# Optimization experiments

Hardware: AMD Instinct MI355X
Metric: run time of the kernel (lower is better)

The kernel has to match this reference:

```python
import jax, jax.numpy as jnp
import numpy as np
import math

H, C = 16, 4


def _clustering(x, alv, mu, log_var, log_prior, mi_estimation):
    # x: [B,h,L,D], alv: [B,h,L], mu/log_var: [h or 1, C, D], log_prior: [h or 1, C]
    B, Hh, L, D = x.shape
    z = x  # eval mode: no reparameterization noise
    zd = z[:, :, :, None, :]                       # [B,h,L,1,D]
    mu_b = mu[:, None, :, :]                       # [h,1,C,D]
    lv = log_var[:, None, :, :]
    var = jnp.exp(lv)
    lp = jax.nn.log_softmax(log_prior, axis=-1)    # [h,C]
    mse = (zd - mu_b) ** 2 / var                   # [B,h,L,C,D]
    log_pdf = -0.5 * mse.sum(-1) - 0.5 * lv.sum(-1) - D * math.pi  # [B,h,L,C]
    log_pdf = log_pdf + lp[:, None, :]
    shift = jax.lax.stop_gradient(log_pdf.max(axis=-1, keepdims=True))
    log_probs = jax.nn.log_softmax(log_pdf - shift + 5.0, axis=-1)
    cp = jnp.exp(log_probs)                        # cluster probs [B,h,L,C]
    lp_b = jnp.broadcast_to(lp[None, :, None, :], log_probs.shape)
    # F.kl_div(log_probs, prior) = prior * (log prior - log_probs)
    kl = (jnp.exp(lp_b) * (lp_b - log_probs)).sum(-1).mean(axis=(1, 2))
    alv5 = alv[:, :, :, None, None]
    avar = jnp.exp(alv5)
    kl = kl + 0.5 * (cp * (mse + avar / var + lv).sum(-1)).sum(-1).mean(axis=(1, 2))
    kl = kl - 0.5 * ((1.0 + alv5).sum(-1) * D).mean(axis=(1, 2, 3))
    eye = jnp.eye(L, dtype=x.dtype)
    div = jnp.einsum('bhqc,bhkc->bhqk', cp, cp)
    div = ((div - eye) ** 2) * (eye * 1.25 + (1.0 - eye) * 0.75)
    div_loss = div.mean(axis=(1, 2, 3))
    if mi_estimation:
        pdf = jnp.exp(log_pdf - jax.lax.stop_gradient(log_pdf.max())).sum(-1, keepdims=True)
        w = cp * pdf
        mi_probs = w / jnp.maximum(w.sum(axis=2, keepdims=True), 1e-6)  # L1 normalize over L
        mi_p = jnp.minimum(jnp.einsum('bilc,bjlc->blij', mi_probs, cp), 1.0)
        mask_h = 1.0 - jnp.eye(Hh, dtype=x.dtype)
        mi_loss = -(jnp.log(1.0 - mi_p + 1e-6) * mask_h).mean(axis=(1, 2, 3)) * 10.0
        aff = jnp.einsum('bhqc,bhkc->bhqk', cp, cp)
        diag = jnp.diagonal(jax.nn.log_softmax(aff, axis=-1), axis1=2, axis2=3)
        mi_loss = mi_loss - diag.mean(axis=(1, 2))
    else:
        mi_loss = jnp.zeros_like(kl)
    return z, cp, kl, div_loss, mi_loss


def _forward(query, key, value, Wq, bq, Wk, bk, Wv, bv, Wo, bo, Wsem, bsem,
             Whead, bhead, tok_mu, tok_log_var, tok_log_prior,
             head_mu, head_log_var, head_log_prior):
    B, L, D = query.shape
    Dk = D // H
    q = query @ Wq + bq
    k = key @ Wk + bk
    v = value @ Wv + bv
    alv = (q @ Wsem + bsem).transpose(0, 2, 1)                 # [B,H,L]
    qh = q.reshape(B, L, H, Dk).transpose(0, 2, 1, 3)          # [B,H,L,Dk]
    z, cp_q, kl_q, div_q, _ = _clustering(qh, alv, tok_mu, tok_log_var, tok_log_prior, False)
    kh = k.reshape(B, L, H, Dk).transpose(0, 2, 1, 3)
    vh = v.reshape(B, L, H, Dk).transpose(0, 2, 1, 3)
    cluster_mask = jnp.einsum('bhqc,bhkc->bhqk', cp_q, cp_q)   # token-cluster affinity mask
    scores = jnp.einsum('bhqd,bhkd->bhqk', z, kh) / math.sqrt(Dk)
    attn = jax.nn.softmax(scores, axis=-1) * cluster_mask
    attn = attn / (attn.sum(axis=-1, keepdims=True) + 1e-6)
    ctx = jnp.einsum('bhqk,bhkd->bhqd', attn, vh)              # [B,H,L,Dk]
    ctx_f = ctx.transpose(0, 2, 1, 3).reshape(B, L, D)
    alv_h = (ctx_f @ Whead + bhead).transpose(0, 2, 1)         # [B,H,L]
    _, cp_h, kl_h, div_h, mi = _clustering(ctx, alv_h, head_mu, head_log_var, head_log_prior, True)
    out = ctx_f @ Wo + bo
    return out, attn.mean(axis=1), kl_q + kl_h, div_q + div_h, mi


def setup_inputs() -> dict:
    key = jax.random.key(0)
    ks = jax.random.split(key, 12)
    B, L, D = 8, 512, 1024
    Dk = D // H
    s = 1.0 / math.sqrt(D)
    f32 = jnp.float32
    inp = {
        'query': jax.random.normal(ks[0], (B, L, D), f32),
        'key': jax.random.normal(ks[1], (B, L, D), f32),
        'value': jax.random.normal(ks[2], (B, L, D), f32),
        'Wq': jax.random.normal(ks[3], (D, D), f32) * s, 'bq': jnp.zeros((D,), f32),
        'Wk': jax.random.normal(ks[4], (D, D), f32) * s, 'bk': jnp.zeros((D,), f32),
        'Wv': jax.random.normal(ks[5], (D, D), f32) * s, 'bv': jnp.zeros((D,), f32),
        'Wo': jax.random.normal(ks[6], (D, D), f32) * s, 'bo': jnp.zeros((D,), f32),
        'Wsem': jax.random.normal(ks[7], (D, H), f32) * s, 'bsem': jnp.zeros((H,), f32),
        'Whead': jax.random.normal(ks[8], (D, H), f32) * s, 'bhead': jnp.zeros((H,), f32),
        'tok_mu': jax.random.normal(ks[9], (H, C, Dk), f32) * 0.1,
        'tok_log_var': jnp.zeros((H, C, Dk), f32),
        'tok_log_prior': jnp.full((H, C), math.log(1.0 / C), f32),
        'head_mu': jax.random.normal(ks[10], (1, C, Dk), f32) * 0.1,
        'head_log_var': jnp.zeros((1, C, Dk), f32),
        'head_log_prior': jnp.full((1, C), math.log(1.0 / C), f32),
    }
    return inp


def reference(query, key, value, Wq, bq, Wk, bk, Wv, bv, Wo, bo, Wsem, bsem,
              Whead, bhead, tok_mu, tok_log_var, tok_log_prior,
              head_mu, head_log_var, head_log_prior):
    return _forward(query, key, value, Wq, bq, Wk, bk, Wv, bv, Wo, bo, Wsem, bsem,
                    Whead, bhead, tok_mu, tok_log_var, tok_log_prior,
                    head_mu, head_log_var, head_log_prior)
```

## Files before the change

### kernel.cpp

```cpp
#include <hip/hip_runtime.h>
#include <math.h>

#define BB 8
#define LL 512
#define DD 1024
#define HH 16
#define CC 4
#define DK 64
#define NEG_DPI 201.06192982974676f

typedef __attribute__((ext_vector_type(8))) short short8;
typedef __attribute__((ext_vector_type(4))) float floatx4;
typedef __attribute__((ext_vector_type(8))) unsigned short u16x8;
typedef __attribute__((ext_vector_type(4))) unsigned short u16x4;

__device__ inline float block_sum256(float v, float* s_red) {
    int t = threadIdx.x;
    s_red[t] = v; __syncthreads();
    for (int off = 128; off > 0; off >>= 1) {
        if (t < off) s_red[t] += s_red[t + off];
        __syncthreads();
    }
    float r = s_red[0]; __syncthreads();
    return r;
}
__device__ inline float block_max256(float v, float* s_red) {
    int t = threadIdx.x;
    s_red[t] = v; __syncthreads();
    for (int off = 128; off > 0; off >>= 1) {
        if (t < off) s_red[t] = fmaxf(s_red[t], s_red[t + off]);
        __syncthreads();
    }
    float r = s_red[0]; __syncthreads();
    return r;
}
__device__ inline unsigned int fenc(float f) {
    unsigned int b = __float_as_uint(f);
    return (b & 0x80000000u) ? ~b : (b | 0x80000000u);
}
__device__ inline float fdec(unsigned int u) {
    return (u & 0x80000000u) ? __uint_as_float(u ^ 0x80000000u) : __uint_as_float(~u);
}
__device__ inline unsigned short f2bf(float x) {
    unsigned int u = __float_as_uint(x);
    return (unsigned short)((u + 0x7FFFu + ((u >> 16) & 1u)) >> 16);
}
__device__ inline unsigned short f2bf_cvt(float x) {
    __bf16 b = (__bf16)x;
    return __builtin_bit_cast(unsigned short, b);
}
__device__ inline float bf2f(unsigned short h) {
    return __uint_as_float((unsigned int)h << 16);
}
__device__ inline void split8(const float4 x, const float4 y, u16x8& h, u16x8& l) {
    float c[8] = {x.x, x.y, x.z, x.w, y.x, y.y, y.z, y.w};
    unsigned short hb[8];
#pragma unroll
    for (int j = 0; j < 8; j++) { hb[j] = f2bf_cvt(c[j]); h[j] = hb[j]; }
#pragma unroll
    for (int j = 0; j < 8; j++) c[j] = c[j] - bf2f(hb[j]);
#pragma unroll
    for (int j = 0; j < 8; j++) l[j] = f2bf_cvt(c[j]);
}

__global__ __launch_bounds__(256)
void wconv4(const float* __restrict__ W0, const float* __restrict__ W1,
            const float* __restrict__ W2, const float* __restrict__ W3,
            unsigned short* __restrict__ Tbase) {
    __shared__ float tile[64][65];
    int z = blockIdx.z;
    const float* W = (z == 0) ? W0 : (z == 1) ? W1 : (z == 2) ? W2 : W3;
    const size_t WS = (size_t)DD * DD;
    unsigned short* Th = Tbase + (size_t)z * 2 * WS;
    unsigned short* Tl = Th + WS;
    int t = threadIdx.x;
    int n0 = blockIdx.x * 64, k0 = blockIdx.y * 64;
    int r = t >> 4, c4 = (t & 15) * 4;
#pragma unroll
    for (int rr = 0; rr < 64; rr += 16) {
        float4 v = *(const float4*)&W[(size_t)(k0 + r + rr) * DD + n0 + c4];
        tile[r + rr][c4 + 0] = v.x; tile[r + rr][c4 + 1] = v.y;
        tile[r + rr][c4 + 2] = v.z; tile[r + rr][c4 + 3] = v.w;
    }
    __syncthreads();
    int rn = t >> 2, kg = (t & 3) * 16;
    u16x8 oh[2], ol[2];
#pragma unroll
    for (int j = 0; j < 16; j++) {
        float x = tile[kg + j][rn];
        unsigned short hb = f2bf(x);
        oh[j >> 3][j & 7] = hb;
        ol[j >> 3][j & 7] = f2bf(x - bf2f(hb));
    }
    size_t o = (size_t)(n0 + rn) * DD + k0 + kg;
    *(u16x8*)&Th[o] = oh[0]; *(u16x8*)&Th[o + 8] = oh[1];
    *(u16x8*)&Tl[o] = ol[0]; *(u16x8*)&Tl[o + 8] = ol[1];
}

template<int AFP32>
__device__ __forceinline__
void gemm_body(const float* __restrict__ Af,
               const unsigned short* __restrict__ Ah, const unsigned short* __restrict__ Al,
               const unsigned short* __restrict__ Bh, const unsigned short* __restrict__ Bl,
               const float* __restrict__ bias, float* __restrict__ C,
               unsigned short* __restrict__ Ch, unsigned short* __restrict__ Cl,
               int m0, int n0) {
    __shared__ unsigned short sAh[128 * 32];
    __shared__ unsigned short sAl[128 * 32];
    __shared__ unsigned short sBh[128 * 32];
    __shared__ unsigned short sBl[128 * 32];
    int t = threadIdx.x;
    int lane = t & 63, w = t >> 6;
    int wm = w >> 1, wn = w & 1;
    int lm = lane & 15, quad = lane >> 4;
    int srow = t >> 1, sk = (t & 1) * 16;

    const float* gAf = AFP32 ? (Af + (size_t)(m0 + srow) * DD + sk) : nullptr;
    const unsigned short* gAh = AFP32 ? nullptr : (Ah + (size_t)(m0 + srow) * DD + sk);
    const unsigned short* gAl = AFP32 ? nullptr : (Al + (size_t)(m0 + srow) * DD + sk);
    const unsigned short* gBh = Bh + (size_t)(n0 + srow) * DD + sk;
    const unsigned short* gBl = Bl + (size_t)(n0 + srow) * DD + sk;
    int f = (srow >> 1) & 3;
    int s0 = (t & 1) * 2;
    int ws0 = srow * 32 + ((s0 ^ f) * 8);
    int ws1 = srow * 32 + (((s0 | 1) ^ f) * 8);

    floatx4 acc[4][4] = {};
    u16x8 a0, a1, a2, a3, b0, b1, b2, b3;
    b0 = *(const u16x8*)(gBh);     b1 = *(const u16x8*)(gBh + 8);
    b2 = *(const u16x8*)(gBl);     b3 = *(const u16x8*)(gBl + 8);
    if (AFP32) {
        float4 f0 = *(const float4*)(gAf);
        float4 f1 = *(const float4*)(gAf + 4);
        float4 f2 = *(const float4*)(gAf + 8);
        float4 f3 = *(const float4*)(gAf + 12);
        split8(f0, f1, a0, a2);
        split8(f2, f3, a1, a3);
    } else {
        a0 = *(const u16x8*)(gAh);     a1 = *(const u16x8*)(gAh + 8);
        a2 = *(const u16x8*)(gAl);     a3 = *(const u16x8*)(gAl + 8);
    }

    for (int kt = 0; kt < 32; kt++) {
        __syncthreads();
        *(u16x8*)&sAh[ws0] = a0; *(u16x8*)&sAh[ws1] = a1;
        *(u16x8*)&sAl[ws0] = a2; *(u16x8*)&sAl[ws1] = a3;
        *(u16x8*)&sBh[ws0] = b0; *(u16x8*)&sBh[ws1] = b1;
        *(u16x8*)&sBl[ws0] = b2; *(u16x8*)&sBl[ws1] = b3;
        __syncthreads();
        if (kt < 31) {
            int kb = (kt + 1) * 32;
            b0 = *(const u16x8*)(gBh + kb); b1 = *(const u16x8*)(gBh + kb + 8);
            b2 = *(const u16x8*)(gBl + kb); b3 = *(const u16x8*)(gBl + kb + 8);
            if (AFP32) {
                float4 f0 = *(const float4*)(gAf + kb);
                float4 f1 = *(const float4*)(gAf + kb + 4);
                float4 f2 = *(const float4*)(gAf + kb + 8);
                float4 f3 = *(const float4*)(gAf + kb + 12);
                split8(f0, f1, a0, a2);
                split8(f2, f3, a1, a3);
            } else {
                a0 = *(const u16x8*)(gAh + kb); a1 = *(const u16x8*)(gAh + kb + 8);
                a2 = *(const u16x8*)(gAl + kb); a3 = *(const u16x8*)(gAl + kb + 8);
            }
        }

        short8 bhf[4], blf[4];
#pragma unroll
        for (int j = 0; j < 4; j++) {
            int nrow = wn * 64 + j * 16 + lm;
            int nb = nrow * 32 + ((quad ^ ((nrow >> 1) & 3)) * 8);
            bhf[j] = *(const short8*)&sBh[nb];
            blf[j] = *(const short8*)&sBl[nb];
        }
#pragma unroll
        for (int i = 0; i < 4; i++) {
            int arow = wm * 64 + i * 16 + lm;
            int ab = arow * 32 + ((quad ^ ((arow >> 1) & 3)) * 8);
            short8 ah = *(const short8*)&sAh[ab];
            short8 al = *(const short8*)&sAl[ab];
#pragma unroll
            for (int j = 0; j < 4; j++) {
                acc[i][j] = __builtin_amdgcn_mfma_f32_16x16x32_bf16(ah, bhf[j], acc[i][j], 0, 0, 0);
                acc[i][j] = __builtin_amdgcn_mfma_f32_16x16x32_bf16(ah, blf[j], acc[i][j], 0, 0, 0);
                acc[i][j] = __builtin_amdgcn_mfma_f32_16x16x32_bf16(al, bhf[j], acc[i][j], 0, 0, 0);
            }
        }
    }
#pragma unroll
    for (int i = 0; i < 4; i++) {
#pragma unroll
        for (int j = 0; j < 4; j++) {
            int n = n0 + wn * 64 + j * 16 + lm;
            float bv = bias[n];
#pragma unroll
            for (int r = 0; r < 4; r++) {
                int m = m0 + wm * 64 + i * 16 + quad * 4 + r;
                size_t idx = (size_t)m * DD + n;
                float val = acc[i][j][r] + bv;
                if (C) C[idx] = val;
                if (Ch) {
                    unsigned short hb = f2bf_cvt(val);
                    Ch[idx] = hb;
                    Cl[idx] = f2bf_cvt(val - bf2f(hb));
                }
            }
        }
    }
}

__global__ __launch_bounds__(256)
void mfma_gemm_bias(const float* __restrict__ Af,
                    const unsigned short* __restrict__ Bh, const unsigned short* __restrict__ Bl,
                    const float* __restrict__ bias, float* __restrict__ C) {
    int id = blockIdx.x;
    int xcd = id & 7, s = id >> 3;
    int y = xcd * 4 + (s >> 3);
    int x = s & 7;
    gemm_body<1>(Af, nullptr, nullptr, Bh, Bl, bias, C, nullptr, nullptr, y * 128, x * 128);
}

__global__ __launch_bounds__(256)
void mfma_gemm_qkv(const float* __restrict__ qin, const float* __restrict__ kin,
                   const float* __restrict__ vin, const unsigned short* __restrict__ wbase,
                   const float* __restrict__ bq, const float* __restrict__ bk,
                   const float* __restrict__ bv, float* __restrict__ Cq,
                   unsigned short* __restrict__ obase) {
    int id = blockIdx.x;
    int xcd = id & 7, s = id >> 3;
    int p = xcd * 12 + (s >> 3);
    int x = s & 7;
    int z = p >> 5;
    int y = p & 31;
    const size_t NB = (size_t)BB * LL * DD;
    const size_t WS = (size_t)DD * DD;
    const float* Af = (z == 0) ? qin : (z == 1) ? kin : vin;
    const unsigned short* Bh = wbase + (size_t)z * 2 * WS;
    const float* bias = (z == 0) ? bq : (z == 1) ? bk : bv;
    float* C = (z == 0) ? Cq : nullptr;
    unsigned short* Ch = obase + (size_t)z * 2 * NB;
    gemm_body<1>(Af, nullptr, nullptr, Bh, Bh + WS, bias, C, Ch, Ch + NB, y * 128, x * 128);
}

__global__ __launch_bounds__(256)
void vt_prep2(const unsigned short* __restrict__ voh, const unsigned short* __restrict__ vol,
              unsigned short* __restrict__ vth, unsigned short* __restrict__ vtl) {
    __shared__ unsigned short tile[128 * 68];
    int t = threadIdx.x;
    int which = blockIdx.x & 1;
    int l0 = (blockIdx.x >> 1) * 128, h = blockIdx.y, b = blockIdx.z;
    const unsigned short* src = which ? vol : voh;
    unsigned short* dst = which ? vtl : vth;
#pragma unroll
    for (int i = 0; i < 8; i++) {
        int u = t + i * 256;
        int l = u >> 4, c4 = (u & 15) * 4;
        u16x4 v4 = *(const u16x4*)&src[((size_t)(b * LL + l0 + l)) * DD + h * DK + c4];
        tile[l * 68 + c4 + 0] = v4[0]; tile[l * 68 + c4 + 1] = v4[1];
        tile[l * 68 + c4 + 2] = v4[2]; tile[l * 68 + c4 + 3] = v4[3];
    }
    __syncthreads();
    size_t ob = ((size_t)(b * HH + h)) * DK * LL;
#pragma unroll
    for (int i = 0; i < 8; i++) {
        int u = t + i * 256;
        int d = u >> 5, lq = (u & 31) * 4;
        u16x4 o;
#pragma unroll
        for (int j = 0; j < 4; j++) o[j] = tile[(lq + j) * 68 + d];
        *(u16x4*)&dst[ob + (size_t)d * LL + l0 + lq] = o;
    }
}

__global__ __launch_bounds__(256)
void alv_gemm(const float* __restrict__ A, const float* __restrict__ Wp,
              const float* __restrict__ bias, float* __restrict__ alv) {
    __shared__ float As[16][65];
    __shared__ float Ws[64][17];
    int t = threadIdx.x;
    int m0 = blockIdx.x * 16;
    int r = t >> 4, hh = t & 15;
    float acc = 0.f;
    for (int kt = 0; kt < 16; kt++) {
        __syncthreads();
#pragma unroll
        for (int i = 0; i < 4; i++) {
            int e = t + i * 256;
            int rr = e >> 6, kk = e & 63;
            As[rr][kk] = A[(size_t)(m0 + rr) * DD + kt * 64 + kk];
        }
#pragma unroll
        for (int i = 0; i < 4; i++) {
            int e = t + i * 256;
            int kk = e >> 4, h2 = e & 15;
            Ws[kk][h2] = Wp[(size_t)(kt * 64 + kk) * HH + h2];
        }
        __syncthreads();
#pragma unroll
        for (int kk = 0; kk < 64; kk++) acc += As[r][kk] * Ws[kk][hh];
    }
    int m = m0 + r;
    int b = m >> 9, l = m & 511;
    alv[(size_t)(b * HH + hh) * LL + l] = acc + bias[hh];
}

__global__ __launch_bounds__(256)
void cluster_kernel(const float* __restrict__ zsrc, const float* __restrict__ alv,
                    const float* __restrict__ mu, const float* __restrict__ logvar,
                    const float* __restrict__ logprior,
                    float* __restrict__ cp_out, float* __restrict__ lpdf_out,
                    unsigned int* __restrict__ maxenc, float* __restrict__ kl_out,
                    int isHead) {
    __shared__ float s_mu[CC * DK], s_iv[CC * DK], s_lv[CC * DK];
    __shared__ float s_slv[CC], s_siv[CC], s_lp[CC];
    __shared__ float s_red[256];
    int t = threadIdx.x;
    int tile = blockIdx.x & 1;
    int bh = blockIdx.x >> 1;
    int h = bh & (HH - 1), b = bh >> 4;
    int hm = isHead ? 0 : h;

    {
        float m = mu[hm * CC * DK + t];
        float lv = logvar[hm * CC * DK + t];
        s_mu[t] = m; s_lv[t] = lv; s_iv[t] = expf(-lv);
    }
    __syncthreads();
    if (t < CC) {
        float slv = 0.f, siv = 0.f;
        for (int d = 0; d < DK; d++) { slv += s_lv[t * DK + d]; siv += s_iv[t * DK + d]; }
        s_slv[t] = slv; s_siv[t] = siv;
    }
    if (t == CC) {
        float x[CC];
        float m = -1e30f;
        for (int c = 0; c < CC; c++) { x[c] = logprior[hm * CC + c]; m = fmaxf(m, x[c]); }
        float se = 0.f;
        for (int c = 0; c < CC; c++) se += expf(x[c] - m);
        float lse = m + logf(se);
        for (int c = 0; c < CC; c++) s_lp[c] = x[c] - lse;
    }
    __syncthreads();

    int l = tile * 256 + t;
    const float* zp = zsrc + ((size_t)(b * LL + l)) * DD + h * DK;
    float acc[CC] = {0.f, 0.f, 0.f, 0.f};
    for (int d = 0; d < DK; d += 4) {
        float4 z4 = *(const float4*)(zp + d);
#pragma unroll
        for (int c = 0; c < CC; c++) {
            float d0 = z4.x - s_mu[c * DK + d];     acc[c] += d0 * d0 * s_iv[c * DK + d];
            float d1 = z4.y - s_mu[c * DK + d + 1]; acc[c] += d1 * d1 * s_iv[c * DK + d + 1];
            float d2 = z4.z - s_mu[c * DK + d + 2]; acc[c] += d2 * d2 * s_iv[c * DK + d + 2];
            float d3 = z4.w - s_mu[c * DK + d + 3]; acc[c] += d3 * d3 * s_iv[c * DK + d + 3];
        }
    }
    float lpdf[CC];
#pragma unroll
    for (int c = 0; c < CC; c++)
        lpdf[c] = -0.5f * acc[c] - 0.5f * s_slv[c] - NEG_DPI + s_lp[c];
    float m = fmaxf(fmaxf(lpdf[0], lpdf[1]), fmaxf(lpdf[2], lpdf[3]));
    float se = 0.f;
#pragma unroll
    for (int c = 0; c < CC; c++) se += expf(lpdf[c] - m);
    float lse = m + logf(se);
    float lprob[CC], cpv[CC];
    size_t idx = ((size_t)(bh * LL + l)) * CC;
#pragma unroll
    for (int c = 0; c < CC; c++) {
        lprob[c] = lpdf[c] - lse;
        cpv[c] = expf(lprob[c]);
        cp_out[idx + c] = cpv[c];
    }
    if (isHead) {
#pragma unroll
        for (int c = 0; c < CC; c++) lpdf_out[idx + c] = lpdf[c];
    }
    float alvv = alv[(size_t)bh * LL + l];
    float avar = expf(alvv);
    float t1 = 0.f, t2 = 0.f;
#pragma unroll
    for (int c = 0; c < CC; c++) {
        t1 += expf(s_lp[c]) * (s_lp[c] - lprob[c]);
        t2 += cpv[c] * (acc[c] + avar * s_siv[c] + s_slv[c]);
    }
    float klv = t1 + 0.5f * t2 - 0.5f * (float)DK * (1.0f + alvv);
    float tot = block_sum256(klv, s_red);
    if (t == 0) atomicAdd(kl_out + b, tot * (1.0f / (HH * LL)));
    if (isHead) {
        float mt = block_max256(m, s_red);
        if (t == 0) atomicMax(maxenc, fenc(mt));
    }
}

__global__ __launch_bounds__(256)
void pairstats_kernel(const float* __restrict__ cp, float* __restrict__ div_out,
                      float* __restrict__ mi_out, int isHead) {
    __shared__ float s_cp[LL * CC];
    __shared__ float s_red[256];
    int t = threadIdx.x;
    int bh = blockIdx.x >> 3;
    int seg = blockIdx.x & 7;
    int b = bh >> 4;
    const float* base = cp + (size_t)bh * LL * CC;
#pragma unroll
    for (int i = 0; i < 2; i++) {
        int e = t + i * 256;
        *(float4*)&s_cp[e * 4] = *(const float4*)&base[e * 4];
    }
    __syncthreads();

    int q = seg * 64 + (t >> 2);
    int ln = t & 3;
    float4 cq = *(float4*)&s_cp[q * 4];
    float divacc = 0.f, m = -1e30f, s = 0.f, selfdot = 0.f;
    for (int k = ln; k < LL; k += 4) {
        float4 ck = *(float4*)&s_cp[k * 4];
        float dot = cq.x * ck.x + cq.y * ck.y + cq.z * ck.z + cq.w * ck.w;
        float del = (k == q) ? 1.f : 0.f;
        float dd = dot - del;
        divacc += dd * dd * (0.75f + 0.5f * del);
        if (isHead) {
            if (dot > m) { s = s * expf(m - dot) + 1.f; m = dot; }
            else         { s += expf(dot - m); }
            if (k == q) selfdot = dot;
        }
    }
#pragma unroll
    for (int off = 1; off <= 2; off <<= 1) divacc += __shfl_xor(divacc, off, 64);
    float diag = 0.f;
    if (isHead) {
#pragma unroll
        for (int off = 1; off <= 2; off <<= 1) {
            float om = __shfl_xor(m, off, 64);
            float os = __shfl_xor(s, off, 64);
            float nm = fmaxf(m, om);
            s = s * expf(m - nm) + os * expf(om - nm);
            m = nm;
        }
#pragma unroll
        for (int off = 1; off <= 2; off <<= 1) selfdot += __shfl_xor(selfdot, off, 64);
        diag = selfdot - (m + logf(s));
    }
    float dtot = block_sum256(ln == 0 ? divacc : 0.f, s_red);
    if (t == 0) atomicAdd(div_out + b, dtot * (1.0f / ((float)HH * LL * LL)));
    if (isHead) {
        float gtot = block_sum256(ln == 0 ? diag : 0.f, s_red);
        if (t == 0) atomicAdd(mi_out + b, -gtot * (1.0f / (HH * LL)));
    }
}

__global__ __launch_bounds__(256)
void attn3_kernel(const unsigned short* __restrict__ qoh, const unsigned short* __restrict__ qol,
                  const unsigned short* __restrict__ koh, const unsigned short* __restrict__ kol,
                  const unsigned short* __restrict__ vth, const unsigned short* __restrict__ vtl,
                  const float* __restrict__ cpq,
                  float* __restrict__ ctxf,
                  float* __restrict__ attn_h, int h0) {
    __shared__ __align__(16) char sbuf[33280];
    __shared__ float s_inv[16];
    float* S = (float*)sbuf;
    unsigned short* Ph = (unsigned short*)sbuf;
    unsigned short* Pl = Ph + 16 * 520;

    int t = threadIdx.x;
    int id = blockIdx.x;
    int xcd = id & 7;
    int sid = id >> 3;
    int qt = sid & 31;
    int combo = ((sid >> 5) << 3) | xcd;
    int hl = combo & 7;
    int b = combo >> 3;
    int h = h0 + hl;
    int q0 = qt * 16;
    int lane = t & 63, w = t >> 6;
    int lm = lane & 15, quad = lane >> 4;
    int bh = b * HH + h;

    size_t qbase = ((size_t)(b * LL + q0 + lm)) * DD + h * DK + quad * 8;
    short8 qah0 = *(const short8*)(qoh + qbase);
    short8 qah1 = *(const short8*)(qoh + qbase + 32);
    short8 qal0 = *(const short8*)(qol + qbase);
    short8 qal1 = *(const short8*)(qol + qbase + 32);

    floatx4 sa[8] = {};
#pragma unroll
    for (int j = 0; j < 8; j++) {
        int n0 = w * 128 + j * 16;
        size_t kbase = ((size_t)(b * LL + n0 + lm)) * DD + h * DK + quad * 8;
        short8 kbh0 = *(const short8*)(koh + kbase);
        short8 kbh1 = *(const short8*)(koh + kbase + 32);
        short8 kbl0 = *(const short8*)(kol + kbase);
        short8 kbl1 = *(const short8*)(kol + kbase + 32);
        sa[j] = __builtin_amdgcn_mfma_f32_16x16x32_bf16(qah0, kbh0, sa[j], 0, 0, 0);
        sa[j] = __builtin_amdgcn_mfma_f32_16x16x32_bf16(qah1, kbh1, sa[j], 0, 0, 0);
        sa[j] = __builtin_amdgcn_mfma_f32_16x16x32_bf16(qah0, kbl0, sa[j], 0, 0, 0);
        sa[j] = __builtin_amdgcn_mfma_f32_16x16x32_bf16(qah1, kbl1, sa[j], 0, 0, 0);
        sa[j] = __builtin_amdgcn_mfma_f32_16x16x32_bf16(qal0, kbh0, sa[j], 0, 0, 0);
        sa[j] = __builtin_amdgcn_mfma_f32_16x16x32_bf16(qal1, kbh1, sa[j], 0, 0, 0);
    }
#pragma unroll
    for (int j = 0; j < 8; j++) {
        int kc = w * 128 + j * 16 + lm;
#pragma unroll
        for (int r = 0; r < 4; r++)
            S[(quad * 4 + r) * 516 + kc] = sa[j][r] * 0.125f;
    }
    __syncthreads();

    {
        int r = t >> 4, ln = t & 15;
        const float4* cpb = (const float4*)(cpq + (size_t)bh * LL * CC);
        float m = -1e30f;
        for (int k = ln; k < LL; k += 16) m = fmaxf(m, S[r * 516 + k]);
#pragma unroll
        for (int off = 8; off > 0; off >>= 1) m = fmaxf(m, __shfl_xor(m, off, 16));
        float4 cq = cpb[q0 + r];
        float Z = 0.f, Sm = 0.f;
        for (int k = ln; k < LL; k += 16) {
            float e = expf(S[r * 516 + k] - m);
            float4 ck = cpb[k];
            float mask = cq.x * ck.x + cq.y * ck.y + cq.z * ck.z + cq.w * ck.w;
            float a = e * mask;
            Z += e; Sm += a;
            S[r * 516 + k] = a;
        }
#pragma unroll
        for (int off = 8; off > 0; off >>= 1) {
            Z += __shfl_xor(Z, off, 16);
            Sm += __shfl_xor(Sm, off, 16);
        }
        if (ln == 0) s_inv[r] = 1.f / (Sm + 1e-6f * Z);
    }
    __syncthreads();

    float4 pv[8];
#pragma unroll
    for (int i = 0; i < 8; i++) {
        int e = t + i * 256;
        int r2 = e >> 7, k4 = (e & 127) * 4;
        float4 p = *(float4*)&S[r2 * 516 + k4];
        float inv = s_inv[r2];
        p.x *= inv; p.y *= inv; p.z *= inv; p.w *= inv;
        pv[i] = p;
        *(float4*)&attn_h[(((size_t)((b * 8 + hl) * LL + q0 + r2)) * LL) + k4] = p;
    }
    __syncthreads();
#pragma unroll
    for (int i = 0; i < 8; i++) {
        int e = t + i * 256;
        int r2 = e >> 7, k4 = (e & 127) * 4;
        float c[4] = {pv[i].x, pv[i].y, pv[i].z, pv[i].w};
        u16x4 hv, lv;
#pragma unroll
        for (int j = 0; j < 4; j++) {
            unsigned short hb = f2bf(c[j]);
            hv[j] = hb;
            lv[j] = f2bf(c[j] - bf2f(hb));
        }
        *(u16x4*)&Ph[r2 * 520 + k4] = hv;
        *(u16x4*)&Pl[r2 * 520 + k4] = lv;
    }
    __syncthreads();

    int dn = w * 16 + lm;
    const unsigned short* vrh = vth + ((size_t)bh * DK + dn) * LL;
    const unsigned short* vrl = vtl + ((size_t)bh * DK + dn) * LL;
    floatx4 ca = {};
#pragma unroll
    for (int kc = 0; kc < 16; kc++) {
        int kb = kc * 32 + quad * 8;
        short8 pah = *(const short8*)&Ph[lm * 520 + kb];
        short8 pal = *(const short8*)&Pl[lm * 520 + kb];
        short8 vbh = *(const short8*)(vrh + kb);
        short8 vbl = *(const short8*)(vrl + kb);
        ca = __builtin_amdgcn_mfma_f32_16x16x32_bf16(pah, vbh, ca, 0, 0, 0);
        ca = __builtin_amdgcn_mfma_f32_16x16x32_bf16(pah, vbl, ca, 0, 0, 0);
        ca = __builtin_amdgcn_mfma_f32_16x16x32_bf16(pal, vbh, ca, 0, 0, 0);
    }
#pragma unroll
    for (int r = 0; r < 4; r++)
        ctxf[((size_t)(b * LL + q0 + quad * 4 + r)) * DD + h * DK + dn] = ca[r];
}

__global__ __launch_bounds__(256)
void attn_reduce(const float* __restrict__ attn_h, float* __restrict__ attn_out,
                 int accumulate) {
    int e = blockIdx.x * 256 + threadIdx.x;
    int b = e >> 16;
    int rem = e & 65535;
    float4 s = {0.f, 0.f, 0.f, 0.f};
#pragma unroll
    for (int hl = 0; hl < 8; hl++) {
        float4 v = ((const float4*)attn_h)[(((size_t)(b * 8 + hl)) << 16) + rem];
        s.x += v.x; s.y += v.y; s.z += v.z; s.w += v.w;
    }
    float4* o = (float4*)attn_out + (((size_t)b) << 16) + rem;
    const float sc = 1.0f / (float)HH;
    float4 prev = {0.f, 0.f, 0.f, 0.f};
    if (accumulate) prev = *o;
    prev.x += s.x * sc; prev.y += s.y * sc; prev.z += s.z * sc; prev.w += s.w * sc;
    *o = prev;
}

__global__ __launch_bounds__(256)
void wsum_kernel(const float* __restrict__ lpdf, const float* __restrict__ cp,
                 const unsigned int* __restrict__ maxenc,
                 float* __restrict__ pdf_out, float* __restrict__ wsum_out) {
    __shared__ float s_red[256];
    int t = threadIdx.x;
    int bh = blockIdx.x;
    float M = fdec(*maxenc);
    float a[CC] = {0.f, 0.f, 0.f, 0.f};
    for (int li = 0; li < 2; li++) {
        int l = t + li * 256;
        size_t idx = ((size_t)bh * LL + l) * CC;
        float p0 = expf(lpdf[idx + 0] - M);
        float p1 = expf(lpdf[idx + 1] - M);
        float p2 = expf(lpdf[idx + 2] - M);
        float p3 = expf(lpdf[idx + 3] - M);
        float pd = p0 + p1 + p2 + p3;
        pdf_out[(size_t)bh * LL + l] = pd;
        a[0] += cp[idx + 0] * pd; a[1] += cp[idx + 1] * pd;
        a[2] += cp[idx + 2] * pd; a[3] += cp[idx + 3] * pd;
    }
#pragma unroll
    for (int c = 0; c < CC; c++) {
        float tot = block_sum256(a[c], s_red);
        if (t == 0) wsum_out[bh * CC + c] = tot;
    }
}

__global__ __launch_bounds__(256)
void mi_kernel(const float* __restrict__ cp, const float* __restrict__ pdf,
               const float* __restrict__ wsum, float* __restrict__ mi_out) {
    __shared__ float s_q[HH * CC];
    __shared__ float s_c[HH * CC];
    __shared__ float s_red[256];
    int t = threadIdx.x;
    int b = blockIdx.x >> 9;
    int l = blockIdx.x & 511;
    if (t < HH * CC) {
        int i = t >> 2, c = t & 3;
        float cpv = cp[((size_t)(b * HH + i) * LL + l) * CC + c];
        s_c[t] = cpv;
        float w = cpv * pdf[(size_t)(b * HH + i) * LL + l];
        float ws = wsum[(b * HH + i) * CC + c];
        s_q[t] = w / fmaxf(ws, 1e-6f);
    }
    __syncthreads();
    int i = t >> 4, j = t & 15;
    float sdot = 0.f;
#pragma unroll
    for (int c = 0; c < CC; c++) sdot += s_q[i * 4 + c] * s_c[j * 4 + c];
    float mi_p = fminf(sdot, 1.f);
    float val = (i != j) ? logf(1.f - mi_p + 1e-6f) : 0.f;
    float tot = block_sum256(val, s_red);
    if (t == 0) atomicAdd(mi_out + b, -10.f * tot * (1.0f / ((float)LL * HH * HH)));
}

extern "C" void kernel_launch(void* const* d_in, const int* in_sizes, int n_in,
                              void* d_out, int out_size, void* d_ws, size_t ws_size,
                              hipStream_t stream) {
    (void)in_sizes; (void)n_in; (void)out_size; (void)ws_size;
    const float* query  = (const float*)d_in[0];
    const float* key    = (const float*)d_in[1];
    const float* value  = (const float*)d_in[2];
    const float* Wq     = (const float*)d_in[3];
    const float* bq     = (const float*)d_in[4];
    const float* Wk     = (const float*)d_in[5];
    const float* bk     = (const float*)d_in[6];
    const float* Wv     = (const float*)d_in[7];
    const float* bv     = (const float*)d_in[8];
    const float* Wo     = (const float*)d_in[9];
    const float* bo     = (const float*)d_in[10];
    const float* Wsem   = (const float*)d_in[11];
    const float* bsem   = (const float*)d_in[12];
    const float* Whead  = (const float*)d_in[13];
    const float* bhead  = (const float*)d_in[14];
    const float* tokmu  = (const float*)d_in[15];
    const float* toklv  = (const float*)d_in[16];
    const float* toklp  = (const float*)d_in[17];
    const float* headmu = (const float*)d_in[18];
    const float* headlv = (const float*)d_in[19];
    const float* headlp = (const float*)d_in[20];

    float* ws   = (float*)d_ws;
    const size_t NBLD = (size_t)BB * LL * DD;
    float* q    = ws;
    float* ctxf = ws + NBLD;
    float* alvq = ws + 2 * NBLD;
    float* alvh = alvq + (size_t)BB * HH * LL;
    float* cpq  = alvh + (size_t)BB * HH * LL;
    float* cph  = cpq + (size_t)BB * HH * LL * CC;
    float* lpdfh= cph + (size_t)BB * HH * LL * CC;
    float* pdfb = lpdfh + (size_t)BB * HH * LL * CC;
    float* wsumb= pdfb + (size_t)BB * HH * LL;
    unsigned int* maxenc = (unsigned int*)(wsumb + (size_t)BB * HH * CC);
    float* attn_h = (float*)(maxenc + 4);

    unsigned short* us = (unsigned short*)(attn_h + (size_t)BB * 8 * LL * LL);
    const size_t WSZ = (size_t)DD * DD;
    unsigned short* qoh = us;
    unsigned short* qol = qoh + NBLD;
    unsigned short* koh = qol + NBLD;
    unsigned short* kol = koh + NBLD;
    unsigned short* voh = kol + NBLD;
    unsigned short* vol = voh + NBLD;
    unsigned short* vth = vol + NBLD;
    unsigned short* vtl = vth + NBLD;
    unsigned short* wqh = vtl + NBLD;
    unsigned short* woh = wqh + 6 * WSZ;
    unsigned short* wol = woh + WSZ;

    float* out      = (float*)d_out;
    float* attn_out = out + NBLD;
    float* kl_out   = attn_out + (size_t)BB * LL * LL;
    float* div_out  = kl_out + BB;
    float* mi_out   = div_out + BB;

    hipMemsetAsync(kl_out, 0, 3 * BB * sizeof(float), stream);
    hipMemsetAsync(maxenc, 0, sizeof(unsigned int), stream);

    wconv4<<<dim3(16, 16, 4), 256, 0, stream>>>(Wq, Wk, Wv, Wo, wqh);

    mfma_gemm_qkv<<<dim3(768), 256, 0, stream>>>(
        query, key, value, wqh, bq, bk, bv, q, qoh);

    vt_prep2<<<dim3(2 * LL / 128, HH, BB), 256, 0, stream>>>(voh, vol, vth, vtl);

    alv_gemm<<<BB * LL / 16, 256, 0, stream>>>(q, Wsem, bsem, alvq);
    cluster_kernel<<<BB * HH * 2, 256, 0, stream>>>(q, alvq, tokmu, toklv, toklp,
                                                    cpq, nullptr, nullptr, kl_out, 0);
    pairstats_kernel<<<BB * HH * 8, 256, 0, stream>>>(cpq, div_out, nullptr, 0);

    for (int h0 = 0; h0 < HH; h0 += 8) {
        attn3_kernel<<<dim3(2048), 256, 0, stream>>>(
            qoh, qol, koh, kol, vth, vtl, cpq, ctxf, attn_h, h0);
        attn_reduce<<<BB * LL * LL / 4 / 256, 256, 0, stream>>>(
            attn_h, attn_out, h0 > 0 ? 1 : 0);
    }

    alv_gemm<<<BB * LL / 16, 256, 0, stream>>>(ctxf, Whead, bhead, alvh);
    cluster_kernel<<<BB * HH * 2, 256, 0, stream>>>(ctxf, alvh, headmu, headlv, headlp,
                                                    cph, lpdfh, maxenc, kl_out, 1);
    pairstats_kernel<<<BB * HH * 8, 256, 0, stream>>>(cph, div_out, mi_out, 1);
    wsum_kernel<<<BB * HH, 256, 0, stream>>>(lpdfh, cph, maxenc, pdfb, wsumb);
    mi_kernel<<<BB * LL, 256, 0, stream>>>(cph, pdfb, wsumb, mi_out);
    mfma_gemm_bias<<<dim3(256), 256, 0, stream>>>(
        ctxf, woh, wol, bo, out);
}
```

Baseline: 737.2 us.

## Replace per-head attention staging and reduce kernel with float atomics

Removes the per-head attention staging buffer and the separate reduction kernel. The attention kernel now runs all 16 heads in one launch and atomically adds each scaled probability into a zero-initialised head-averaged output. Block-to-XCD mapping now keys on batch. This cuts the staging write and re-read traffic, but introduces four scalar float atomics per element with contention across 16 heads, plus a memset and nondeterministic summation order.

```diff
diff --git a/kernel.cpp b/kernel.cpp
--- a/kernel.cpp
+++ b/kernel.cpp
@@ -456,7 +456,7 @@
                   const unsigned short* __restrict__ vth, const unsigned short* __restrict__ vtl,
                   const float* __restrict__ cpq,
                   float* __restrict__ ctxf,
-                  float* __restrict__ attn_h, int h0) {
+                  float* __restrict__ attn_out) {
     __shared__ __align__(16) char sbuf[33280];
     __shared__ float s_inv[16];
     float* S = (float*)sbuf;
@@ -465,13 +465,10 @@
 
     int t = threadIdx.x;
     int id = blockIdx.x;
-    int xcd = id & 7;
+    int b = id & 7;
     int sid = id >> 3;
     int qt = sid & 31;
-    int combo = ((sid >> 5) << 3) | xcd;
-    int hl = combo & 7;
-    int b = combo >> 3;
-    int h = h0 + hl;
+    int h = sid >> 5;
     int q0 = qt * 16;
     int lane = t & 63, w = t >> 6;
     int lm = lane & 15, quad = lane >> 4;
@@ -535,6 +532,7 @@
     __syncthreads();
 
     float4 pv[8];
+    const float sc = 1.0f / (float)HH;
 #pragma unroll
     for (int i = 0; i < 8; i++) {
         int e = t + i * 256;
@@ -543,7 +541,11 @@
         float inv = s_inv[r2];
         p.x *= inv; p.y *= inv; p.z *= inv; p.w *= inv;
         pv[i] = p;
-        *(float4*)&attn_h[(((size_t)((b * 8 + hl) * LL + q0 + r2)) * LL) + k4] = p;
+        float* dst = attn_out + ((size_t)(b * LL + q0 + r2)) * LL + k4;
+        unsafeAtomicAdd(dst + 0, p.x * sc);
+        unsafeAtomicAdd(dst + 1, p.y * sc);
+        unsafeAtomicAdd(dst + 2, p.z * sc);
+        unsafeAtomicAdd(dst + 3, p.w * sc);
     }
     __syncthreads();
 #pragma unroll
@@ -581,26 +583,6 @@
 #pragma unroll
     for (int r = 0; r < 4; r++)
         ctxf[((size_t)(b * LL + q0 + quad * 4 + r)) * DD + h * DK + dn] = ca[r];
-}
-
-__global__ __launch_bounds__(256)
-void attn_reduce(const float* __restrict__ attn_h, float* __restrict__ attn_out,
-                 int accumulate) {
-    int e = blockIdx.x * 256 + threadIdx.x;
-    int b = e >> 16;
-    int rem = e & 65535;
-    float4 s = {0.f, 0.f, 0.f, 0.f};
-#pragma unroll
-    for (int hl = 0; hl < 8; hl++) {
-        float4 v = ((const float4*)attn_h)[(((size_t)(b * 8 + hl)) << 16) + rem];
-        s.x += v.x; s.y += v.y; s.z += v.z; s.w += v.w;
-    }
-    float4* o = (float4*)attn_out + (((size_t)b) << 16) + rem;
-    const float sc = 1.0f / (float)HH;
-    float4 prev = {0.f, 0.f, 0.f, 0.f};
-    if (accumulate) prev = *o;
-    prev.x += s.x * sc; prev.y += s.y * sc; prev.z += s.z * sc; prev.w += s.w * sc;
-    *o = prev;
 }
 
 __global__ __launch_bounds__(256)
@@ -697,9 +679,9 @@
     float* pdfb = lpdfh + (size_t)BB * HH * LL * CC;
     float* wsumb= pdfb + (size_t)BB * HH * LL;
     unsigned int* maxenc = (unsigned int*)(wsumb + (size_t)BB * HH * CC);
-    float* attn_h = (float*)(maxenc + 4);
-
-    unsigned short* us = (unsigned short*)(attn_h + (size_t)BB * 8 * LL * LL);
+    float* scr3 = (float*)(maxenc + 4);
+
+    unsigned short* us = (unsigned short*)(scr3 + (size_t)BB * 8 * LL * LL);
     const size_t WSZ = (size_t)DD * DD;
     unsigned short* qoh = us;
     unsigned short* qol = qoh + NBLD;
@@ -721,6 +703,7 @@
 
     hipMemsetAsync(kl_out, 0, 3 * BB * sizeof(float), stream);
     hipMemsetAsync(maxenc, 0, sizeof(unsigned int), stream);
+    hipMemsetAsync(attn_out, 0, (size_t)BB * LL * LL * sizeof(float), stream);
 
     wconv4<<<dim3(16, 16, 4), 256, 0, stream>>>(Wq, Wk, Wv, Wo, wqh);
 
@@ -734,12 +717,8 @@
                                                     cpq, nullptr, nullptr, kl_out, 0);
     pairstats_kernel<<<BB * HH * 8, 256, 0, stream>>>(cpq, div_out, nullptr, 0);
 
-    for (int h0 = 0; h0 < HH; h0 += 8) {
-        attn3_kernel<<<dim3(2048), 256, 0, stream>>>(
-            qoh, qol, koh, kol, vth, vtl, cpq, ctxf, attn_h, h0);
-        attn_reduce<<<BB * LL * LL / 4 / 256, 256, 0, stream>>>(
-            attn_h, attn_out, h0 > 0 ? 1 : 0);
-    }
+    attn3_kernel<<<dim3(4096), 256, 0, stream>>>(
+        qoh, qol, koh, kol, vth, vtl, cpq, ctxf, attn_out);
 
     alv_gemm<<<BB * LL / 16, 256, 0, stream>>>(ctxf, Whead, bhead, alvh);
     cluster_kernel<<<BB * HH * 2, 256, 0, stream>>>(ctxf, alvh, headmu, headlv, headlp,
```

Result: slower. 1.018 ms (+38.1%).
